# Kernel tuning notes

Measured on AMD Instinct MI355X. Metric: run time of the kernel, lower is better.

The kernel has to match this reference:

```python
import jax, jax.numpy as jnp
import numpy as np

H_HEADS = 4
C_HID = 128
N_GENE = 50000
N_DIS = 25000
F_GENE = 512
F_DIS = 256
E1 = 150000
E2 = 150000
BN_EPS = 1e-5


def _encode(x, W, b, gamma, beta):
    # Linear -> ReLU -> (dropout off) -> BatchNorm1d (train-mode batch stats, biased var)
    h = jax.nn.relu(x @ W + b)
    mu = h.mean(axis=0)
    var = h.var(axis=0)
    return gamma * (h - mu) * jax.lax.rsqrt(var + BN_EPS) + beta


def _with_self_loops(src, dst, n_loop):
    # PyG GATConv: remove_self_loops (mask src==dst) then add_self_loops(num_nodes=min(Ns,Nd))
    loop = jnp.arange(n_loop, dtype=src.dtype)
    mask = jnp.concatenate([src != dst, jnp.ones((n_loop,), bool)])
    return jnp.concatenate([src, loop]), jnp.concatenate([dst, loop]), mask


def _gat(x_src, x_dst, src, dst, mask, Ws, Wd, a_s, a_d, bias, n_dst):
    H, C = a_s.shape
    xs = (x_src @ Ws).reshape(-1, H, C)  # [Ns,H,C]
    xd = (x_dst @ Wd).reshape(-1, H, C)  # [Nd,H,C]
    ls = jnp.sum(xs * a_s, axis=-1)      # [Ns,H]
    ld = jnp.sum(xd * a_d, axis=-1)      # [Nd,H]
    logits = jax.nn.leaky_relu(ls[src] + ld[dst], 0.2)  # [E,H]
    logits = jnp.where(mask[:, None], logits, jnp.asarray(-1e30, logits.dtype))
    m = jax.ops.segment_max(logits, dst, num_segments=n_dst)
    m = jnp.where(jnp.isfinite(m), m, 0.0)  # empty segments -> -inf fill
    p = jnp.exp(logits - m[dst]) * mask[:, None]
    denom = jax.ops.segment_sum(p, dst, num_segments=n_dst)[dst]
    alpha = p / jnp.where(denom > 0, denom, 1.0)  # softmax per destination
    out = jax.ops.segment_sum(alpha[:, :, None] * xs[src], dst, num_segments=n_dst)
    return out.mean(axis=1) + bias  # concat=False: mean over heads


def _forward(x_gene, x_dis, e1_src, e1_dst, e2_src, e2_dst,
             Wg, bg, gg, betag, Wd, bd, gd, betad,
             W1s, W1d, a1s, a1d, b1, W2s, W2d, a2s, a2d, b2):
    gene = _encode(x_gene, Wg, bg, gg, betag)
    dis = _encode(x_dis, Wd, bd, gd, betad)
    # relation 1: Disease -> Gene (bipartite); self loops use min(N_dis, N_gene)
    s1, d1, m1 = _with_self_loops(e1_src, e1_dst, min(N_DIS, N_GENE))
    gene = gene + _gat(dis, gene, s1, d1, m1, W1s, W1d, a1s, a1d, b1, N_GENE)
    # relation 2: Gene -> Gene (uses updated gene features)
    s2, d2, m2 = _with_self_loops(e2_src, e2_dst, N_GENE)
    gene = gene + _gat(gene, gene, s2, d2, m2, W2s, W2d, a2s, a2d, b2, N_GENE)
    # output_layer is skipped: gene dim (128) != hidden*heads (512)
    return gene, dis


def setup_inputs() -> dict:
    key = jax.random.key(0)
    ks = jax.random.split(key, 24)
    H, C = H_HEADS, C_HID

    def glorot(k, shape):
        fan = shape[0] + shape[-1]
        return jax.random.normal(k, shape, jnp.float32) * np.sqrt(2.0 / fan).astype(np.float32)

    return {
        'x_gene': jax.random.normal(ks[0], (N_GENE, F_GENE), jnp.float32),
        'x_dis': jax.random.normal(ks[1], (N_DIS, F_DIS), jnp.float32),
        'e1_src': jax.random.randint(ks[2], (E1,), 0, N_DIS, jnp.int32),
        'e1_dst': jax.random.randint(ks[3], (E1,), 0, N_GENE, jnp.int32),
        'e2_src': jax.random.randint(ks[4], (E2,), 0, N_GENE, jnp.int32),
        'e2_dst': jax.random.randint(ks[5], (E2,), 0, N_GENE, jnp.int32),
        'Wg': glorot(ks[6], (F_GENE, C)), 'bg': jnp.zeros(C), 'gg': jnp.ones(C), 'betag': jnp.zeros(C),
        'Wd': glorot(ks[7], (F_DIS, C)), 'bd': jnp.zeros(C), 'gd': jnp.ones(C), 'betad': jnp.zeros(C),
        'W1s': glorot(ks[8], (C, H * C)), 'W1d': glorot(ks[9], (C, H * C)),
        'a1s': glorot(ks[10], (H, C)), 'a1d': glorot(ks[11], (H, C)), 'b1': jnp.zeros(C),
        'W2s': glorot(ks[12], (C, H * C)), 'W2d': glorot(ks[13], (C, H * C)),
        'a2s': glorot(ks[14], (H, C)), 'a2d': glorot(ks[15], (H, C)), 'b2': jnp.zeros(C),
    }


def reference(x_gene, x_dis, e1_src, e1_dst, e2_src, e2_dst,
              Wg, bg, gg, betag, Wd, bd, gd, betad,
              W1s, W1d, a1s, a1d, b1, W2s, W2d, a2s, a2d, b2):
    return _forward(x_gene, x_dis, e1_src, e1_dst, e2_src, e2_dst,
                    Wg, bg, gg, betag, Wd, bd, gd, betad,
                    W1s, W1d, a1s, a1d, b1, W2s, W2d, a2s, a2d, b2)
```

## Files before the change

kernel.cpp:

```cpp
#include <hip/hip_runtime.h>
#include <hip/hip_bf16.h>
#include <math.h>

#define N_GENE 50000
#define N_DIS  25000
#define F_GENE 512
#define F_DIS  256
#define E_EDGES 150000
#define BN_EPS 1e-5f

typedef unsigned short u16;
typedef unsigned int u32;
typedef short s16x8 __attribute__((ext_vector_type(8)));
typedef float f32x4 __attribute__((ext_vector_type(4)));

__device__ __forceinline__ u16 f2bf(float f) {
    union { float f; unsigned u; } c; c.f = f;
    unsigned u = c.u;
    unsigned rounding = 0x7FFFu + ((u >> 16) & 1u);
    return (u16)((u + rounding) >> 16);
}
__device__ __forceinline__ void load_bf16x8(const u16* p, float* f) {
    uint4 q = *reinterpret_cast<const uint4*>(p);
    unsigned w0 = q.x, w1 = q.y, w2 = q.z, w3 = q.w;
    f[0] = __uint_as_float(w0 << 16); f[1] = __uint_as_float(w0 & 0xffff0000u);
    f[2] = __uint_as_float(w1 << 16); f[3] = __uint_as_float(w1 & 0xffff0000u);
    f[4] = __uint_as_float(w2 << 16); f[5] = __uint_as_float(w2 & 0xffff0000u);
    f[6] = __uint_as_float(w3 << 16); f[7] = __uint_as_float(w3 & 0xffff0000u);
}

__device__ __forceinline__ void gload_lds16(const u16* g, u16* l) {
    __builtin_amdgcn_global_load_lds(
        (const __attribute__((address_space(1))) u32*)g,
        (__attribute__((address_space(3))) u32*)l, 16, 0, 0);
}

__device__ __forceinline__ void pack_one(const float* __restrict__ W, u16* __restrict__ Bp,
                                         int K, int N, int i) {
    int K8 = K >> 3;
    int n = i / K8, ko = i - n * K8;
    int k0 = ko * 8;
    int nt = n >> 4, mr = n & 15, kc = k0 >> 5, quad = (k0 >> 3) & 3;
    u16 tmp[8];
#pragma unroll
    for (int j = 0; j < 8; j++) tmp[j] = f2bf(W[(size_t)(k0 + j) * N + n]);
    *reinterpret_cast<uint4*>(&Bp[((size_t)(nt * (K >> 5) + kc) * 64 + quad * 16 + mr) * 8]) =
        *reinterpret_cast<const uint4*>(tmp);
}

__global__ void prep(const float* __restrict__ Wg, const float* __restrict__ Wd,
                     const float* __restrict__ W1s, const float* __restrict__ W2s,
                     u16* __restrict__ Wgt, u16* __restrict__ Wdt,
                     u16* __restrict__ W1st, u16* __restrict__ W2st,
                     float* __restrict__ stats_g, float* __restrict__ stats_d,
                     int* __restrict__ deg1, int* __restrict__ deg2,
                     const float* __restrict__ W1d, const float* __restrict__ a1d,
                     const float* __restrict__ W2d, const float* __restrict__ a2d,
                     float* __restrict__ weff) {
    int i = blockIdx.x * 256 + threadIdx.x;
    if (i < 8192) { pack_one(Wg, Wgt, 512, 128, i); return; }
    i -= 8192;
    if (i < 4096) { pack_one(Wd, Wdt, 256, 128, i); return; }
    i -= 4096;
    if (i < 8192) { pack_one(W1s, W1st, 128, 512, i); return; }
    i -= 8192;
    if (i < 8192) { pack_one(W2s, W2st, 128, 512, i); return; }
    i -= 8192;
    if (i < 256) { stats_g[i] = 0.f; return; }
    i -= 256;
    if (i < 256) { stats_d[i] = 0.f; return; }
    i -= 256;
    if (i < N_GENE) { deg1[i] = 0; return; }
    i -= N_GENE;
    if (i < N_GENE) { deg2[i] = 0; return; }
    i -= N_GENE;
    if (i < 1024) {
        int rel = i >> 9, tt = i & 511;
        int h = tt >> 7, k = tt & 127;
        const float* Wp = rel ? W2d : W1d;
        const float* ap = rel ? a2d : a1d;
        float s = 0.f;
        for (int c = 0; c < 128; c++) s += Wp[k * 512 + h * 128 + c] * ap[h * 128 + c];
        weff[rel * 512 + h * 128 + k] = s;
    }
}

template <int K, bool A_FRAG, bool RELU_BIAS, bool OUT_BF16, bool FUSE_STATS, bool FUSE_LS>
__global__ __launch_bounds__(256) void gemm_lds(const void* __restrict__ Ap,
                                                const u16* __restrict__ Bp,
                                                const float* __restrict__ bias,
                                                void* __restrict__ outp, int M, int NFULL,
                                                float* __restrict__ stats,
                                                const float* __restrict__ as_,
                                                float* __restrict__ ls_out) {
    constexpr int KC = K / 32;
    constexpr int CK = 2;
    constexpr int NCH = KC / CK;
    __shared__ u16 Bs[2][8 * CK * 64 * 8];
    __shared__ float sstat[256];
    const int wave = threadIdx.x >> 6;
    const int lane = threadIdx.x & 63;
    const int mrow = lane & 15;
    const int quad = lane >> 4;
    const int m0 = (blockIdx.x * 4 + wave) * 16;
    const int n0 = blockIdx.y * 128;
    const int arow = (m0 + mrow < M) ? m0 + mrow : M - 1;
    const int rt = (m0 >> 4) < ((M + 15) >> 4) ? (m0 >> 4) : ((M + 15) >> 4) - 1;
    const u16* bslab = Bp + (size_t)(n0 >> 4) * KC * 512;

    if constexpr (FUSE_STATS) sstat[threadIdx.x] = 0.f;

    f32x4 acc[8];
#pragma unroll
    for (int t = 0; t < 8; t++) acc[t] = (f32x4){0.f, 0.f, 0.f, 0.f};

    struct ARegs { float4 f[2 * CK]; s16x8 s[CK]; };
    ARegs A0, A1;

    auto stageB = [&](int c, int b) {
#pragma unroll
        for (int q = 0; q < 2 * CK; q++) {
            int fi = wave * 2 * CK + q;
            int t = fi / CK, kcp = fi % CK;
            const u16* g = bslab + ((size_t)(t * KC + c * CK + kcp) * 64 + lane) * 8;
            gload_lds16(g, &Bs[b][(size_t)fi * 512]);
        }
    };
    auto loadA = [&](int c, ARegs& A) {
        if constexpr (A_FRAG) {
#pragma unroll
            for (int kcp = 0; kcp < CK; kcp++)
                A.s[kcp] = *reinterpret_cast<const s16x8*>(
                    (const u16*)Ap + ((size_t)(rt * KC + c * CK + kcp) * 64 + lane) * 8);
        } else {
#pragma unroll
            for (int kcp = 0; kcp < CK; kcp++) {
                const float* ap = (const float*)Ap + (size_t)arow * K + (c * CK + kcp) * 32 + quad * 8;
                A.f[2 * kcp]     = *reinterpret_cast<const float4*>(ap);
                A.f[2 * kcp + 1] = *reinterpret_cast<const float4*>(ap + 4);
            }
        }
    };
    auto compute = [&](const u16* Bsb, const ARegs& A) {
#pragma unroll
        for (int kcp = 0; kcp < CK; kcp++) {
            s16x8 af;
            if constexpr (A_FRAG) {
                af = A.s[kcp];
            } else {
                const float4 lo = A.f[2 * kcp], hi = A.f[2 * kcp + 1];
                af[0] = (short)f2bf(lo.x); af[1] = (short)f2bf(lo.y);
                af[2] = (short)f2bf(lo.z); af[3] = (short)f2bf(lo.w);
                af[4] = (short)f2bf(hi.x); af[5] = (short)f2bf(hi.y);
                af[6] = (short)f2bf(hi.z); af[7] = (short)f2bf(hi.w);
            }
#pragma unroll
            for (int t = 0; t < 8; t++) {
                const s16x8 bfr = *reinterpret_cast<const s16x8*>(
                    &Bsb[((size_t)(t * CK + kcp) * 64 + lane) * 8]);
                acc[t] = __builtin_amdgcn_mfma_f32_16x16x32_bf16(af, bfr, acc[t], 0, 0, 0);
            }
        }
    };

#define FENCE_N() do { if constexpr (A_FRAG) asm volatile("s_waitcnt vmcnt(6)" ::: "memory"); \
                       else                  asm volatile("s_waitcnt vmcnt(8)" ::: "memory"); } while (0)
#define FENCE_0() asm volatile("s_waitcnt vmcnt(0)" ::: "memory")
#define LGKM0()   asm volatile("s_waitcnt lgkmcnt(0)" ::: "memory")
#define BAR()     asm volatile("s_barrier" ::: "memory")

    stageB(0, 0);
    loadA(0, A0);
    for (int cc = 0; cc < NCH / 2; ++cc) {
        stageB(2 * cc + 1, 1);
        loadA(2 * cc + 1, A1);
        FENCE_N();
        BAR();
        compute(&Bs[0][0], A0);
        LGKM0();
        BAR();
        if (cc + 1 < NCH / 2) {
            stageB(2 * cc + 2, 0);
            loadA(2 * cc + 2, A0);
            FENCE_N();
        } else {
            FENCE_0();
        }
        BAR();
        compute(&Bs[1][0], A1);
        LGKM0();
        BAR();
    }
#undef FENCE_N
#undef FENCE_0
#undef LGKM0
#undef BAR

    float asv[8];
    if constexpr (FUSE_LS) {
        const int h = blockIdx.y;
#pragma unroll
        for (int t = 0; t < 8; t++) asv[t] = as_[h * 128 + t * 16 + mrow];
    }
    float lsp[4] = {0.f, 0.f, 0.f, 0.f};

#pragma unroll
    for (int t = 0; t < 8; t++) {
        int col = n0 + t * 16 + mrow;
        float sv = 0.f, sv2 = 0.f;
#pragma unroll
        for (int r = 0; r < 4; r++) {
            int orow = m0 + quad * 4 + r;
            if (orow < M) {
                float v = acc[t][r];
                if (RELU_BIAS) v = fmaxf(v + bias[col], 0.f);
                if (OUT_BF16)
                    ((u16*)outp)[(size_t)orow * NFULL + col] = f2bf(v);
                else
                    ((float*)outp)[(size_t)orow * NFULL + col] = v;
                if constexpr (FUSE_STATS) { sv += v; sv2 += v * v; }
                if constexpr (FUSE_LS) lsp[r] += v * asv[t];
            }
        }
        if constexpr (FUSE_STATS) {
            sv  += __shfl_xor(sv, 16, 64);  sv  += __shfl_xor(sv, 32, 64);
            sv2 += __shfl_xor(sv2, 16, 64); sv2 += __shfl_xor(sv2, 32, 64);
            if (quad == 0) {
                atomicAdd(&sstat[t * 16 + mrow], sv);
                atomicAdd(&sstat[128 + t * 16 + mrow], sv2);
            }
        }
    }
    if constexpr (FUSE_LS) {
        const int h = blockIdx.y;
#pragma unroll
        for (int r = 0; r < 4; r++) {
            float p = lsp[r];
            p += __shfl_xor(p, 1, 64); p += __shfl_xor(p, 2, 64);
            p += __shfl_xor(p, 4, 64); p += __shfl_xor(p, 8, 64);
            int orow = m0 + quad * 4 + r;
            if (mrow == 0 && orow < M) ls_out[orow * 4 + h] = p;
        }
    }
    if constexpr (FUSE_STATS) {
        __syncthreads();
        atomicAdd(&stats[threadIdx.x], sstat[threadIdx.x]);
    }
}

__global__ void bn_apply(float* __restrict__ X, const float* __restrict__ stats,
                         const float* __restrict__ gamma, const float* __restrict__ beta,
                         u16* __restrict__ mirror, const float* __restrict__ weff,
                         float* __restrict__ ld_out, int M) {
    int i = blockIdx.x * 256 + threadIdx.x;
    if (i >= M * 16) return;
    int row = i >> 4, cg = i & 15;
    float inv_m = 1.0f / (float)M;
    float4 lo = *reinterpret_cast<const float4*>(&X[(size_t)row * 128 + cg * 8]);
    float4 hi = *reinterpret_cast<const float4*>(&X[(size_t)row * 128 + cg * 8 + 4]);
    float v[8] = {lo.x, lo.y, lo.z, lo.w, hi.x, hi.y, hi.z, hi.w};
    u16 mb[8];
#pragma unroll
    for (int e = 0; e < 8; e++) {
        int col = cg * 8 + e;
        float mu = stats[col] * inv_m;
        float var = stats[128 + col] * inv_m - mu * mu;
        v[e] = gamma[col] * (v[e] - mu) * rsqrtf(var + BN_EPS) + beta[col];
        mb[e] = f2bf(v[e]);
    }
    *reinterpret_cast<float4*>(&X[(size_t)row * 128 + cg * 8]) = (float4){v[0], v[1], v[2], v[3]};
    *reinterpret_cast<float4*>(&X[(size_t)row * 128 + cg * 8 + 4]) = (float4){v[4], v[5], v[6], v[7]};
    if (mirror) {
        int kc = cg >> 2, quad = cg & 3, ml = quad * 16 + (row & 15), rt = row >> 4;
        *reinterpret_cast<uint4*>(&mirror[((size_t)(rt * 4 + kc) * 64 + ml) * 8]) =
            *reinterpret_cast<const uint4*>(mb);
    }
    if (ld_out) {
#pragma unroll
        for (int h = 0; h < 4; h++) {
            float p = 0.f;
#pragma unroll
            for (int e = 0; e < 8; e++) p += v[e] * weff[h * 128 + cg * 8 + e];
            p += __shfl_xor(p, 1, 64); p += __shfl_xor(p, 2, 64);
            p += __shfl_xor(p, 4, 64); p += __shfl_xor(p, 8, 64);
            if (cg == 0) ld_out[row * 4 + h] = p;
        }
    }
}

__global__ void count_both(const int* __restrict__ e1s, const int* __restrict__ e1d,
                           const int* __restrict__ e2s, const int* __restrict__ e2d,
                           int* __restrict__ deg1, int* __restrict__ deg2) {
    int i = blockIdx.x * 256 + threadIdx.x;
    if (i < E_EDGES + N_DIS) {
        int d;
        if (i < E_EDGES) { int s = e1s[i]; d = e1d[i]; if (s == d) return; }
        else d = i - E_EDGES;
        atomicAdd(&deg1[d], 1);
        return;
    }
    i -= E_EDGES + N_DIS;
    if (i < E_EDGES + N_GENE) {
        int d;
        if (i < E_EDGES) { int s = e2s[i]; d = e2d[i]; if (s == d) return; }
        else d = i - E_EDGES;
        atomicAdd(&deg2[d], 1);
    }
}

__global__ void block_sum_both(const int* __restrict__ deg1, const int* __restrict__ deg2,
                               int* __restrict__ bsum, int nb) {
    __shared__ int sh[256];
    int rel = blockIdx.x >= nb;
    int blk = rel ? blockIdx.x - nb : blockIdx.x;
    const int* deg = rel ? deg2 : deg1;
    int i = blk * 256 + threadIdx.x;
    sh[threadIdx.x] = (i < N_GENE) ? deg[i] : 0;
    __syncthreads();
    for (int s = 128; s > 0; s >>= 1) {
        if (threadIdx.x < s) sh[threadIdx.x] += sh[threadIdx.x + s];
        __syncthreads();
    }
    if (threadIdx.x == 0) bsum[blockIdx.x] = sh[0];
}

__global__ void scan_bsum_both(int* __restrict__ bsum, int nb,
                               int* __restrict__ offs1, int* __restrict__ offs2) {
    __shared__ int sh[256];
    int* bs = bsum + blockIdx.x * nb;
    int tid = threadIdx.x;
    int v = (tid < nb) ? bs[tid] : 0;
    sh[tid] = v;
    __syncthreads();
    for (int off = 1; off < 256; off <<= 1) {
        int t = (tid >= off) ? sh[tid - off] : 0;
        __syncthreads();
        sh[tid] += t;
        __syncthreads();
    }
    if (tid < nb) bs[tid] = sh[tid] - v;
    if (tid == 255) (blockIdx.x ? offs2 : offs1)[N_GENE] = sh[255];
}

__global__ void scan_final_both(const int* __restrict__ deg1, const int* __restrict__ deg2,
                                const int* __restrict__ bsum, int nb,
                                int* __restrict__ offs1, int* __restrict__ cur1,
                                int* __restrict__ offs2, int* __restrict__ cur2) {
    __shared__ int sh[256];
    int rel = blockIdx.x >= nb;
    int blk = rel ? blockIdx.x - nb : blockIdx.x;
    const int* deg = rel ? deg2 : deg1;
    int* offs = rel ? offs2 : offs1;
    int* cur  = rel ? cur2  : cur1;
    int i = blk * 256 + threadIdx.x, tid = threadIdx.x;
    int v = (i < N_GENE) ? deg[i] : 0;
    sh[tid] = v;
    __syncthreads();
    for (int off = 1; off < 256; off <<= 1) {
        int t = (tid >= off) ? sh[tid - off] : 0;
        __syncthreads();
        sh[tid] += t;
        __syncthreads();
    }
    int ex = bsum[blockIdx.x] + sh[tid] - v;
    if (i < N_GENE) { offs[i] = ex; cur[i] = ex; }
}

__global__ void scatter_both(const int* __restrict__ e1s, const int* __restrict__ e1d,
                             const int* __restrict__ e2s, const int* __restrict__ e2d,
                             int* __restrict__ cur1, int* __restrict__ cur2,
                             int* __restrict__ esrc1, int* __restrict__ esrc2) {
    int i = blockIdx.x * 256 + threadIdx.x;
    if (i < E_EDGES + N_DIS) {
        int s, d;
        if (i < E_EDGES) { s = e1s[i]; d = e1d[i]; if (s == d) return; }
        else { s = i - E_EDGES; d = s; }
        esrc1[atomicAdd(&cur1[d], 1)] = s;
        return;
    }
    i -= E_EDGES + N_DIS;
    if (i < E_EDGES + N_GENE) {
        int s, d;
        if (i < E_EDGES) { s = e2s[i]; d = e2d[i]; if (s == d) return; }
        else { s = i - E_EDGES; d = s; }
        esrc2[atomicAdd(&cur2[d], 1)] = s;
    }
}

__global__ void gat_kernel(const int* __restrict__ offs, const int* __restrict__ esrc,
                           const float* __restrict__ ls, const float* __restrict__ ld,
                           const u16* __restrict__ xs, const float* __restrict__ bias,
                           float* __restrict__ xdst_out, u16* __restrict__ mirror,
                           const float* __restrict__ weff2, float* __restrict__ ld2_out,
                           int n_dst) {
    int wid = (blockIdx.x * blockDim.x + threadIdx.x) >> 6;
    int lane = threadIdx.x & 63;
    if (wid >= n_dst) return;
    int h = lane >> 4;
    int beg = offs[wid], end = offs[wid + 1];
    float ldv = ld[wid * 4 + h];
    float m = -INFINITY;
    for (int j = beg; j < end; j++) {
        int s = esrc[j];
        float l = ls[s * 4 + h] + ldv;
        l = l > 0.f ? l : 0.2f * l;
        m = fmaxf(m, l);
    }
    float denom = 0.f;
    float acc[8] = {0.f, 0.f, 0.f, 0.f, 0.f, 0.f, 0.f, 0.f};
    for (int j = beg; j < end; j++) {
        int s = esrc[j];
        float l = ls[s * 4 + h] + ldv;
        l = l > 0.f ? l : 0.2f * l;
        float p = __expf(l - m);
        denom += p;
        float xv[8];
        load_bf16x8(xs + (size_t)s * 512 + lane * 8, xv);
        #pragma unroll
        for (int k = 0; k < 8; k++) acc[k] += p * xv[k];
    }
    float dinv = denom > 0.f ? 1.f / denom : 1.f;
    #pragma unroll
    for (int k = 0; k < 8; k++) {
        float v = acc[k] * dinv;
        v += __shfl_xor(v, 16, 64);
        v += __shfl_xor(v, 32, 64);
        acc[k] = v * 0.25f;
    }
    if (lane < 16) {
        int c0 = lane * 8;
        float vout[8];
        #pragma unroll
        for (int k = 0; k < 8; k++) {
            vout[k] = xdst_out[(size_t)wid * 128 + c0 + k] + acc[k] + bias[c0 + k];
            xdst_out[(size_t)wid * 128 + c0 + k] = vout[k];
        }
        if (mirror) {
            unsigned pk[4];
            #pragma unroll
            for (int kk = 0; kk < 4; kk++)
                pk[kk] = (unsigned)f2bf(vout[2 * kk]) | ((unsigned)f2bf(vout[2 * kk + 1]) << 16);
            int kc = lane >> 2, quad = lane & 3, ml = quad * 16 + (wid & 15), rt = wid >> 4;
            *reinterpret_cast<uint4*>(&mirror[((size_t)(rt * 4 + kc) * 64 + ml) * 8]) =
                *reinterpret_cast<const uint4*>(pk);
        }
        if (weff2) {
            #pragma unroll
            for (int hh = 0; hh < 4; hh++) {
                float p = 0.f;
                #pragma unroll
                for (int k = 0; k < 8; k++) p += vout[k] * weff2[hh * 128 + c0 + k];
                p += __shfl_xor(p, 1, 64); p += __shfl_xor(p, 2, 64);
                p += __shfl_xor(p, 4, 64); p += __shfl_xor(p, 8, 64);
                if (lane == 0) ld2_out[wid * 4 + hh] = p;
            }
        }
    }
}

static inline int cdiv(int a, int b) { return (a + b - 1) / b; }

extern "C" void kernel_launch(void* const* d_in, const int* in_sizes, int n_in,
                              void* d_out, int out_size, void* d_ws, size_t ws_size,
                              hipStream_t stream) {
    const float* x_gene = (const float*)d_in[0];
    const float* x_dis  = (const float*)d_in[1];
    const int* e1s = (const int*)d_in[2];
    const int* e1d = (const int*)d_in[3];
    const int* e2s = (const int*)d_in[4];
    const int* e2d = (const int*)d_in[5];
    const float *Wg = (const float*)d_in[6],  *bg = (const float*)d_in[7];
    const float *gg = (const float*)d_in[8],  *betag = (const float*)d_in[9];
    const float *Wd = (const float*)d_in[10], *bd = (const float*)d_in[11];
    const float *gd = (const float*)d_in[12], *betad = (const float*)d_in[13];
    const float *W1s = (const float*)d_in[14], *W1d = (const float*)d_in[15];
    const float *a1s = (const float*)d_in[16], *a1d = (const float*)d_in[17];
    const float *b1  = (const float*)d_in[18];
    const float *W2s = (const float*)d_in[19], *W2d = (const float*)d_in[20];
    const float *a2s = (const float*)d_in[21], *a2d = (const float*)d_in[22];
    const float *b2  = (const float*)d_in[23];

    float* gene_f = (float*)d_out;
    float* dis_f  = (float*)d_out + (size_t)N_GENE * 128;

    char* p = (char*)d_ws;
    auto alloc = [&](size_t bytes) {
        char* r = p;
        p += (bytes + 255) & ~(size_t)255;
        return r;
    };
    u16*   xs_buf  = (u16*)  alloc((size_t)N_GENE * 512 * 2);
    u16*   gene_bf = (u16*)  alloc((size_t)cdiv(N_GENE, 16) * 2048 * 2);
    u16*   dis_bf  = (u16*)  alloc((size_t)cdiv(N_DIS, 16) * 2048 * 2);
    float* ls_buf  = (float*)alloc((size_t)N_GENE * 4 * 4);
    float* ld1_buf = (float*)alloc((size_t)N_GENE * 4 * 4);
    float* ld2_buf = (float*)alloc((size_t)N_GENE * 4 * 4);
    float* weff    = (float*)alloc(1024 * 4);
    float* stats_g = (float*)alloc(256 * 4);
    float* stats_d = (float*)alloc(256 * 4);
    int*   deg1    = (int*)  alloc((size_t)N_GENE * 4);
    int*   deg2    = (int*)  alloc((size_t)N_GENE * 4);
    int*   offs1   = (int*)  alloc((size_t)(N_GENE + 1) * 4);
    int*   offs2   = (int*)  alloc((size_t)(N_GENE + 1) * 4);
    int*   cur1    = (int*)  alloc((size_t)N_GENE * 4);
    int*   cur2    = (int*)  alloc((size_t)N_GENE * 4);
    int*   bsum    = (int*)  alloc(512 * 4);
    int*   esrc1   = (int*)  alloc((size_t)(E_EDGES + N_GENE) * 4);
    int*   esrc2   = (int*)  alloc((size_t)(E_EDGES + N_GENE) * 4);
    u16*   Wgt  = (u16*)alloc((size_t)8 * 16 * 512 * 2);
    u16*   Wdt  = (u16*)alloc((size_t)8 * 8 * 512 * 2);
    u16*   W1st = (u16*)alloc((size_t)32 * 4 * 512 * 2);
    u16*   W2st = (u16*)alloc((size_t)32 * 4 * 512 * 2);

    const int NB = cdiv(N_GENE, 256);

    const int PREP_T = 8192 + 4096 + 8192 + 8192 + 256 + 256 + N_GENE + N_GENE + 1024;
    prep<<<cdiv(PREP_T, 256), 256, 0, stream>>>(Wg, Wd, W1s, W2s, Wgt, Wdt, W1st, W2st,
                                                stats_g, stats_d, deg1, deg2,
                                                W1d, a1d, W2d, a2d, weff);
    const int EB = cdiv((E_EDGES + N_DIS) + (E_EDGES + N_GENE), 256);
    count_both<<<EB, 256, 0, stream>>>(e1s, e1d, e2s, e2d, deg1, deg2);
    block_sum_both<<<2 * NB, 256, 0, stream>>>(deg1, deg2, bsum, NB);
    scan_bsum_both<<<2, 256, 0, stream>>>(bsum, NB, offs1, offs2);
    scan_final_both<<<2 * NB, 256, 0, stream>>>(deg1, deg2, bsum, NB, offs1, cur1, offs2, cur2);
    scatter_both<<<EB, 256, 0, stream>>>(e1s, e1d, e2s, e2d, cur1, cur2, esrc1, esrc2);

    gemm_lds<512, false, true, false, true, false><<<dim3(cdiv(N_GENE, 64), 1), 256, 0, stream>>>(
        x_gene, Wgt, bg, gene_f, N_GENE, 128, stats_g, nullptr, nullptr);
    bn_apply<<<cdiv(N_GENE * 16, 256), 256, 0, stream>>>(gene_f, stats_g, gg, betag,
                                                         nullptr, weff, ld1_buf, N_GENE);

    gemm_lds<256, false, true, false, true, false><<<dim3(cdiv(N_DIS, 64), 1), 256, 0, stream>>>(
        x_dis, Wdt, bd, dis_f, N_DIS, 128, stats_d, nullptr, nullptr);
    bn_apply<<<cdiv(N_DIS * 16, 256), 256, 0, stream>>>(dis_f, stats_d, gd, betad,
                                                        dis_bf, nullptr, nullptr, N_DIS);

    gemm_lds<128, true, false, true, false, true><<<dim3(cdiv(N_DIS, 64), 4), 256, 0, stream>>>(
        dis_bf, W1st, nullptr, xs_buf, N_DIS, 512, nullptr, a1s, ls_buf);
    gat_kernel<<<cdiv(N_GENE, 4), 256, 0, stream>>>(offs1, esrc1, ls_buf, ld1_buf, xs_buf, b1,
                                                    gene_f, gene_bf, weff + 512, ld2_buf, N_GENE);

    gemm_lds<128, true, false, true, false, true><<<dim3(cdiv(N_GENE, 64), 4), 256, 0, stream>>>(
        gene_bf, W2st, nullptr, xs_buf, N_GENE, 512, nullptr, a2s, ls_buf);
    gat_kernel<<<cdiv(N_GENE, 4), 256, 0, stream>>>(offs2, esrc2, ls_buf, ld2_buf, xs_buf, b2,
                                                    gene_f, nullptr, nullptr, nullptr, N_GENE);
}
```

Baseline: 476.5 us.

## Load GEMM B fragments straight into registers instead of staging through LDS

The GEMM kernel stops staging the packed weight tiles into shared memory with global_load_lds and barriers. Each wave now loads its own B fragments from global memory into registers, double-buffered with the A fragments. This removes the block-wide barriers, explicit waitcnt fences and LDS traffic. In exchange each of the four waves reloads the same B data, which relies on L1/L2 hits, and the register footprint grows, which may lower occupancy.

```diff
diff --git a/kernel.cpp b/kernel.cpp
--- a/kernel.cpp
+++ b/kernel.cpp
@@ -27,12 +27,6 @@
     f[2] = __uint_as_float(w1 << 16); f[3] = __uint_as_float(w1 & 0xffff0000u);
     f[4] = __uint_as_float(w2 << 16); f[5] = __uint_as_float(w2 & 0xffff0000u);
     f[6] = __uint_as_float(w3 << 16); f[7] = __uint_as_float(w3 & 0xffff0000u);
-}
-
-__device__ __forceinline__ void gload_lds16(const u16* g, u16* l) {
-    __builtin_amdgcn_global_load_lds(
-        (const __attribute__((address_space(1))) u32*)g,
-        (__attribute__((address_space(3))) u32*)l, 16, 0, 0);
 }
 
 __device__ __forceinline__ void pack_one(const float* __restrict__ W, u16* __restrict__ Bp,
@@ -86,7 +80,7 @@
 }
 
 template <int K, bool A_FRAG, bool RELU_BIAS, bool OUT_BF16, bool FUSE_STATS, bool FUSE_LS>
-__global__ __launch_bounds__(256) void gemm_lds(const void* __restrict__ Ap,
+__global__ __launch_bounds__(256) void gemm_reg(const void* __restrict__ Ap,
                                                 const u16* __restrict__ Bp,
                                                 const float* __restrict__ bias,
                                                 void* __restrict__ outp, int M, int NFULL,
@@ -94,15 +88,13 @@
                                                 const float* __restrict__ as_,
                                                 float* __restrict__ ls_out) {
     constexpr int KC = K / 32;
-    constexpr int CK = 2;
-    constexpr int NCH = KC / CK;
-    __shared__ u16 Bs[2][8 * CK * 64 * 8];
     __shared__ float sstat[256];
     const int wave = threadIdx.x >> 6;
     const int lane = threadIdx.x & 63;
     const int mrow = lane & 15;
     const int quad = lane >> 4;
-    const int m0 = (blockIdx.x * 4 + wave) * 16;
+    const int wid = blockIdx.x * 4 + wave;
+    const int m0 = wid * 16;
     const int n0 = blockIdx.y * 128;
     const int arow = (m0 + mrow < M) ? m0 + mrow : M - 1;
     const int rt = (m0 >> 4) < ((M + 15) >> 4) ? (m0 >> 4) : ((M + 15) >> 4) - 1;
@@ -114,87 +106,52 @@
 #pragma unroll
     for (int t = 0; t < 8; t++) acc[t] = (f32x4){0.f, 0.f, 0.f, 0.f};
 
-    struct ARegs { float4 f[2 * CK]; s16x8 s[CK]; };
+    struct BRegs { s16x8 b[8]; };
+    struct ARegs { float4 f[2]; s16x8 s; };
+    BRegs B0, B1;
     ARegs A0, A1;
 
-    auto stageB = [&](int c, int b) {
-#pragma unroll
-        for (int q = 0; q < 2 * CK; q++) {
-            int fi = wave * 2 * CK + q;
-            int t = fi / CK, kcp = fi % CK;
-            const u16* g = bslab + ((size_t)(t * KC + c * CK + kcp) * 64 + lane) * 8;
-            gload_lds16(g, &Bs[b][(size_t)fi * 512]);
-        }
+    auto loadB = [&](int kc, BRegs& B) {
+#pragma unroll
+        for (int t = 0; t < 8; t++)
+            B.b[t] = *reinterpret_cast<const s16x8*>(
+                bslab + ((size_t)(t * KC + kc) * 64 + lane) * 8);
     };
-    auto loadA = [&](int c, ARegs& A) {
+    auto loadA = [&](int kc, ARegs& A) {
         if constexpr (A_FRAG) {
-#pragma unroll
-            for (int kcp = 0; kcp < CK; kcp++)
-                A.s[kcp] = *reinterpret_cast<const s16x8*>(
-                    (const u16*)Ap + ((size_t)(rt * KC + c * CK + kcp) * 64 + lane) * 8);
+            A.s = *reinterpret_cast<const s16x8*>(
+                (const u16*)Ap + ((size_t)(rt * KC + kc) * 64 + lane) * 8);
         } else {
-#pragma unroll
-            for (int kcp = 0; kcp < CK; kcp++) {
-                const float* ap = (const float*)Ap + (size_t)arow * K + (c * CK + kcp) * 32 + quad * 8;
-                A.f[2 * kcp]     = *reinterpret_cast<const float4*>(ap);
-                A.f[2 * kcp + 1] = *reinterpret_cast<const float4*>(ap + 4);
-            }
+            const float* ap = (const float*)Ap + (size_t)arow * K + kc * 32 + quad * 8;
+            A.f[0] = *reinterpret_cast<const float4*>(ap);
+            A.f[1] = *reinterpret_cast<const float4*>(ap + 4);
         }
     };
-    auto compute = [&](const u16* Bsb, const ARegs& A) {
-#pragma unroll
-        for (int kcp = 0; kcp < CK; kcp++) {
-            s16x8 af;
-            if constexpr (A_FRAG) {
-                af = A.s[kcp];
-            } else {
-                const float4 lo = A.f[2 * kcp], hi = A.f[2 * kcp + 1];
-                af[0] = (short)f2bf(lo.x); af[1] = (short)f2bf(lo.y);
-                af[2] = (short)f2bf(lo.z); af[3] = (short)f2bf(lo.w);
-                af[4] = (short)f2bf(hi.x); af[5] = (short)f2bf(hi.y);
-                af[6] = (short)f2bf(hi.z); af[7] = (short)f2bf(hi.w);
-            }
-#pragma unroll
-            for (int t = 0; t < 8; t++) {
-                const s16x8 bfr = *reinterpret_cast<const s16x8*>(
-                    &Bsb[((size_t)(t * CK + kcp) * 64 + lane) * 8]);
-                acc[t] = __builtin_amdgcn_mfma_f32_16x16x32_bf16(af, bfr, acc[t], 0, 0, 0);
-            }
-        }
+    auto compute = [&](const BRegs& B, const ARegs& A) {
+        s16x8 af;
+        if constexpr (A_FRAG) {
+            af = A.s;
+        } else {
+            const float4 lo = A.f[0], hi = A.f[1];
+            af[0] = (short)f2bf(lo.x); af[1] = (short)f2bf(lo.y);
+            af[2] = (short)f2bf(lo.z); af[3] = (short)f2bf(lo.w);
+            af[4] = (short)f2bf(hi.x); af[5] = (short)f2bf(hi.y);
+            af[6] = (short)f2bf(hi.z); af[7] = (short)f2bf(hi.w);
+        }
+#pragma unroll
+        for (int t = 0; t < 8; t++)
+            acc[t] = __builtin_amdgcn_mfma_f32_16x16x32_bf16(af, B.b[t], acc[t], 0, 0, 0);
     };
 
-#define FENCE_N() do { if constexpr (A_FRAG) asm volatile("s_waitcnt vmcnt(6)" ::: "memory"); \
-                       else                  asm volatile("s_waitcnt vmcnt(8)" ::: "memory"); } while (0)
-#define FENCE_0() asm volatile("s_waitcnt vmcnt(0)" ::: "memory")
-#define LGKM0()   asm volatile("s_waitcnt lgkmcnt(0)" ::: "memory")
-#define BAR()     asm volatile("s_barrier" ::: "memory")
-
-    stageB(0, 0);
+    loadB(0, B0);
     loadA(0, A0);
-    for (int cc = 0; cc < NCH / 2; ++cc) {
-        stageB(2 * cc + 1, 1);
-        loadA(2 * cc + 1, A1);
-        FENCE_N();
-        BAR();
-        compute(&Bs[0][0], A0);
-        LGKM0();
-        BAR();
-        if (cc + 1 < NCH / 2) {
-            stageB(2 * cc + 2, 0);
-            loadA(2 * cc + 2, A0);
-            FENCE_N();
-        } else {
-            FENCE_0();
-        }
-        BAR();
-        compute(&Bs[1][0], A1);
-        LGKM0();
-        BAR();
-    }
-#undef FENCE_N
-#undef FENCE_0
-#undef LGKM0
-#undef BAR
+#pragma unroll
+    for (int kc = 0; kc < KC; kc += 2) {
+        if (kc + 1 < KC) { loadB(kc + 1, B1); loadA(kc + 1, A1); }
+        compute(B0, A0);
+        if (kc + 2 < KC) { loadB(kc + 2, B0); loadA(kc + 2, A0); }
+        if (kc + 1 < KC) compute(B1, A1);
+    }
 
     float asv[8];
     if constexpr (FUSE_LS) {
@@ -525,22 +482,22 @@
     scan_final_both<<<2 * NB, 256, 0, stream>>>(deg1, deg2, bsum, NB, offs1, cur1, offs2, cur2);
     scatter_both<<<EB, 256, 0, stream>>>(e1s, e1d, e2s, e2d, cur1, cur2, esrc1, esrc2);
 
-    gemm_lds<512, false, true, false, true, false><<<dim3(cdiv(N_GENE, 64), 1), 256, 0, stream>>>(
+    gemm_reg<512, false, true, false, true, false><<<dim3(cdiv(N_GENE, 64), 1), 256, 0, stream>>>(
         x_gene, Wgt, bg, gene_f, N_GENE, 128, stats_g, nullptr, nullptr);
     bn_apply<<<cdiv(N_GENE * 16, 256), 256, 0, stream>>>(gene_f, stats_g, gg, betag,
                                                          nullptr, weff, ld1_buf, N_GENE);
 
-    gemm_lds<256, false, true, false, true, false><<<dim3(cdiv(N_DIS, 64), 1), 256, 0, stream>>>(
+    gemm_reg<256, false, true, false, true, false><<<dim3(cdiv(N_DIS, 64), 1), 256, 0, stream>>>(
         x_dis, Wdt, bd, dis_f, N_DIS, 128, stats_d, nullptr, nullptr);
     bn_apply<<<cdiv(N_DIS * 16, 256), 256, 0, stream>>>(dis_f, stats_d, gd, betad,
                                                         dis_bf, nullptr, nullptr, N_DIS);
 
-    gemm_lds<128, true, false, true, false, true><<<dim3(cdiv(N_DIS, 64), 4), 256, 0, stream>>>(
+    gemm_reg<128, true, false, true, false, true><<<dim3(cdiv(N_DIS, 64), 4), 256, 0, stream>>>(
         dis_bf, W1st, nullptr, xs_buf, N_DIS, 512, nullptr, a1s, ls_buf);
     gat_kernel<<<cdiv(N_GENE, 4), 256, 0, stream>>>(offs1, esrc1, ls_buf, ld1_buf, xs_buf, b1,
                                                     gene_f, gene_bf, weff + 512, ld2_buf, N_GENE);
 
-    gemm_lds<128, true, false, true, false, true><<<dim3(cdiv(N_GENE, 64), 4), 256, 0, stream>>>(
+    gemm_reg<128, true, false, true, false, true><<<dim3(cdiv(N_GENE, 64), 4), 256, 0, stream>>>(
         gene_bf, W2st, nullptr, xs_buf, N_GENE, 512, nullptr, a2s, ls_buf);
     gat_kernel<<<cdiv(N_GENE, 4), 256, 0, stream>>>(offs2, esrc2, ls_buf, ld2_buf, xs_buf, b2,
                                                     gene_f, nullptr, nullptr, nullptr, N_GENE);
```

New measurement: 494.6 us. +3.8%, slower.
